# Kernel optimization log

Measured on AMD Instinct MI355X. Metric: run time of the kernel, lower is better.

Reference implementation:

```python
import jax, jax.numpy as jnp
import numpy as np

B, A, S, D, OUT = 8, 16384, 2048, 512, 512
REDUCTION = "mean"  # matches init_kwargs


def setup_inputs() -> dict:
    key = jax.random.key(0)
    k1, k2, k3 = jax.random.split(key, 3)
    input_rep = jax.random.normal(k1, (B, A, D), jnp.float32)
    # sorted residue ids per protein (atoms are stored residue-by-residue)
    aa_res_ids = jnp.sort(jax.random.randint(k2, (B, A), 0, S), axis=-1).astype(jnp.int32)
    input_aa_len = jnp.full((B,), A, jnp.int32)
    input_seq_len = jnp.full((B,), S, jnp.int32)
    W = jax.random.normal(k3, (OUT, D), jnp.float32) / np.sqrt(D)
    bias = jnp.zeros((OUT,), jnp.float32)
    return {"input_rep": input_rep, "aa_res_ids": aa_res_ids,
            "input_aa_len": input_aa_len, "input_seq_len": input_seq_len,
            "W": W, "bias": bias}


def _pool(input_rep, aa_res_ids, input_aa_len, input_seq_len):
    # input_rep: [B, A, D]; aa_res_ids: [B, A] in [0, S)
    Bv, Av, Dv = input_rep.shape
    valid = jnp.arange(Av)[None, :] < input_aa_len[:, None]          # [B, A] atoms within aa_len
    seg = jnp.arange(Bv)[:, None] * S + aa_res_ids                   # flatten (b, res_id) -> segment id
    seg = jnp.where(valid, seg, Bv * S)                              # invalid atoms -> dummy segment
    nseg = Bv * S + 1
    seg_f = seg.reshape(-1)
    counts = jax.ops.segment_sum(valid.reshape(-1).astype(input_rep.dtype), seg_f,
                                 num_segments=nseg)[: Bv * S].reshape(Bv, S)
    if REDUCTION == "mean":
        sums = jax.ops.segment_sum(input_rep.reshape(Bv * Av, Dv), seg_f,
                                   num_segments=nseg)[: Bv * S].reshape(Bv, S, Dv)
        pooled = sums / jnp.maximum(counts, 1)[..., None]
    elif REDUCTION == "max":
        vals = jnp.where(valid[..., None], input_rep, -jnp.inf).reshape(Bv * Av, Dv)
        pooled = jax.ops.segment_max(vals, seg_f, num_segments=nseg)[: Bv * S].reshape(Bv, S, Dv)
        pooled = jnp.where((counts > 0)[..., None], pooled, 0.0)
    else:
        raise ValueError("Unsupported reduction method: {}".format(REDUCTION))
    in_seq = jnp.arange(S)[None, :] < input_seq_len[:, None]         # [B, S] positions within seq_len
    filled = (counts > 0) & in_seq                                   # residues that received >=1 atom
    n_fill = filled.sum(axis=1)                                      # [B]
    avg = (pooled * filled[..., None]).sum(axis=1) / jnp.maximum(n_fill, 1)[:, None].astype(input_rep.dtype)
    # unfilled-but-in-range positions get the per-protein average of filled residues; out-of-range stay 0
    out = jnp.where(filled[..., None], pooled,
                    jnp.where(in_seq[..., None], avg[:, None, :], jnp.zeros((), input_rep.dtype)))
    return out


def reference(input_rep, aa_res_ids, input_aa_len, input_seq_len, W, bias):
    out = _pool(input_rep, aa_res_ids, input_aa_len, input_seq_len)  # [B, S, D]
    return out @ W.T + bias                                          # [B, S, OUT]
```

## Files before the change

### kernel.cpp

```cpp
#include <hip/hip_runtime.h>
#include <cstdint>
#include <cstddef>

#define Bv 8
#define Av 16384
#define Sv 2048
#define Dv 512
#define OUTv 512
#define Mv (Bv * Sv)

using u16 = unsigned short;
using f32x4 = __attribute__((ext_vector_type(4))) float;
using bf16x8 = __attribute__((ext_vector_type(8))) short;

__device__ __forceinline__ u16 f2bf(float x) {
  union { float f; uint32_t u; } v; v.f = x;
  uint32_t u = v.u;
  uint32_t r = u + 0x7FFFu + ((u >> 16) & 1u);
  return (u16)(r >> 16);
}
__device__ __forceinline__ float bf2f(u16 h) {
  union { uint32_t u; float f; } v; v.u = ((uint32_t)h) << 16; return v.f;
}

__device__ __forceinline__ void gl_lds16(const void* g, void* s) {
  __builtin_amdgcn_global_load_lds(
      (const __attribute__((address_space(1))) unsigned int*)g,
      (__attribute__((address_space(3))) unsigned int*)s, 16, 0, 0);
}

__global__ __launch_bounds__(256)
void starts_kernel(const int* __restrict__ res_ids, const int* __restrict__ aa_len,
                   int* __restrict__ starts) {
  const int b = blockIdx.y;
  const int a = blockIdx.x * 256 + threadIdx.x;
  int alen = aa_len[b];
  alen = alen < 0 ? 0 : (alen > Av ? Av : alen);
  int* st = starts + b * (Sv + 1);
  if (a >= alen) {
    if (a == 0) {
      for (int s = 0; s <= Sv; ++s) st[s] = 0;
    }
    return;
  }
  const int* ids = res_ids + b * Av;
  const int id = ids[a];
  const int p = (a == 0) ? -1 : ids[a - 1];
  for (int s = p + 1; s <= id; ++s) st[s] = a;
  if (a == alen - 1) {
    for (int s = id + 1; s <= Sv; ++s) st[s] = alen;
  }
}

__global__ __launch_bounds__(128)
void pool_kernel(const float* __restrict__ rep, const int* __restrict__ starts,
                 u16* __restrict__ pooled) {
  const int bs = blockIdx.x;
  const int b = bs >> 11;
  const int s = bs & (Sv - 1);
  const int* st = starts + b * (Sv + 1);
  const int start = st[s];
  const int end = st[s + 1];
  const int cnt = end - start;

  const int t = threadIdx.x;
  float p0 = 0.f, p1 = 0.f, p2 = 0.f, p3 = 0.f;
  float q0 = 0.f, q1 = 0.f, q2 = 0.f, q3 = 0.f;
  float r0 = 0.f, r1 = 0.f, r2 = 0.f, r3 = 0.f;
  float w0 = 0.f, w1 = 0.f, w2 = 0.f, w3 = 0.f;
  const float* base = rep + (size_t)b * Av * Dv + t * 4;
  int a = start;
  for (; a + 4 <= end; a += 4) {
    float4 v0 = *(const float4*)(base + (size_t)(a + 0) * Dv);
    float4 v1 = *(const float4*)(base + (size_t)(a + 1) * Dv);
    float4 v2 = *(const float4*)(base + (size_t)(a + 2) * Dv);
    float4 v3 = *(const float4*)(base + (size_t)(a + 3) * Dv);
    p0 += v0.x; p1 += v0.y; p2 += v0.z; p3 += v0.w;
    q0 += v1.x; q1 += v1.y; q2 += v1.z; q3 += v1.w;
    r0 += v2.x; r1 += v2.y; r2 += v2.z; r3 += v2.w;
    w0 += v3.x; w1 += v3.y; w2 += v3.z; w3 += v3.w;
  }
  for (; a < end; ++a) {
    float4 v = *(const float4*)(base + (size_t)a * Dv);
    p0 += v.x; p1 += v.y; p2 += v.z; p3 += v.w;
  }
  p0 += q0 + r0 + w0; p1 += q1 + r1 + w1; p2 += q2 + r2 + w2; p3 += q3 + r3 + w3;
  const float inv = cnt > 0 ? 1.0f / (float)cnt : 0.0f;
  ushort4 o = { f2bf(p0 * inv), f2bf(p1 * inv), f2bf(p2 * inv), f2bf(p3 * inv) };
  *(ushort4*)(pooled + (size_t)bs * Dv + t * 4) = o;
}

__global__ __launch_bounds__(256)
void wconv_kernel(const float* __restrict__ W, u16* __restrict__ Wb) {
  const int i = (blockIdx.x * 256 + threadIdx.x) * 4;
  float4 v = *(const float4*)(W + i);
  ushort4 o = { f2bf(v.x), f2bf(v.y), f2bf(v.z), f2bf(v.w) };
  *(ushort4*)(Wb + i) = o;
}

__global__ __launch_bounds__(128)
void avg_kernel(const u16* __restrict__ pooled, const int* __restrict__ starts,
                const int* __restrict__ seq_len, float* __restrict__ avg_sum,
                int* __restrict__ n_fill) {
  const int b = blockIdx.x;
  const int chunk = blockIdx.y;
  const int t = threadIdx.x;
  int slen = seq_len[b];
  slen = slen < 0 ? 0 : (slen > Sv ? Sv : slen);
  const int* st = starts + b * (Sv + 1);
  const int s0 = chunk * 16;
  float a0 = 0.f, a1 = 0.f, a2 = 0.f, a3 = 0.f;
  int filled = 0;
  for (int s = s0; s < s0 + 16; ++s) {
    if (s < slen && st[s + 1] - st[s] > 0) {
      ++filled;
      ushort4 v = *(const ushort4*)(pooled + ((size_t)(b * Sv + s)) * Dv + t * 4);
      a0 += bf2f(v.x); a1 += bf2f(v.y); a2 += bf2f(v.z); a3 += bf2f(v.w);
    }
  }
  atomicAdd(&avg_sum[b * Dv + t * 4 + 0], a0);
  atomicAdd(&avg_sum[b * Dv + t * 4 + 1], a1);
  atomicAdd(&avg_sum[b * Dv + t * 4 + 2], a2);
  atomicAdd(&avg_sum[b * Dv + t * 4 + 3], a3);
  if (t == 0 && filled > 0) atomicAdd(&n_fill[b], filled);
}

__global__ __launch_bounds__(64)
void fixup_kernel(u16* __restrict__ pooled, const int* __restrict__ starts,
                  const int* __restrict__ seq_len, const float* __restrict__ avg_sum,
                  const int* __restrict__ n_fill) {
  const int bs = blockIdx.x;
  const int b = bs >> 11;
  const int s = bs & (Sv - 1);
  int slen = seq_len[b];
  slen = slen < 0 ? 0 : (slen > Sv ? Sv : slen);
  const int* st = starts + b * (Sv + 1);
  const int cnt = st[s + 1] - st[s];
  const int t = threadIdx.x;
  if (s >= slen) {
    if (cnt != 0) {
      ushort4 z = {0, 0, 0, 0};
      *(ushort4*)(pooled + (size_t)bs * Dv + t * 8) = z;
      *(ushort4*)(pooled + (size_t)bs * Dv + t * 8 + 4) = z;
    }
    return;
  }
  if (cnt > 0) return;
  const int nf = n_fill[b];
  const float inv = 1.0f / (float)(nf > 0 ? nf : 1);
  float4 v0 = *(const float4*)(avg_sum + b * Dv + t * 8);
  float4 v1 = *(const float4*)(avg_sum + b * Dv + t * 8 + 4);
  ushort4 o0 = { f2bf(v0.x * inv), f2bf(v0.y * inv), f2bf(v0.z * inv), f2bf(v0.w * inv) };
  ushort4 o1 = { f2bf(v1.x * inv), f2bf(v1.y * inv), f2bf(v1.z * inv), f2bf(v1.w * inv) };
  *(ushort4*)(pooled + (size_t)bs * Dv + t * 8) = o0;
  *(ushort4*)(pooled + (size_t)bs * Dv + t * 8 + 4) = o1;
}

#define BM 128
#define BN 128
#define BK 64

__global__ __launch_bounds__(256, 2)
void gemm_kernel(const u16* __restrict__ A, const u16* __restrict__ Bw,
                 const float* __restrict__ bias, float* __restrict__ out) {
  __shared__ alignas(16) u16 As[BM * BK];
  __shared__ alignas(16) u16 Bs[BN * BK];
  const int tid = threadIdx.x;
  const int m0 = blockIdx.x * BM;
  const int n0 = blockIdx.y * BN;
  const int lane = tid & 63;
  const int wave = tid >> 6;
  const int wm = (wave & 1) * 64;
  const int wn = (wave >> 1) * 64;
  const int fr = lane & 15;
  const int fq = lane >> 4;

  f32x4 acc[4][4];
#pragma unroll
  for (int i = 0; i < 4; ++i)
#pragma unroll
    for (int j = 0; j < 4; ++j) acc[i][j] = (f32x4){0.f, 0.f, 0.f, 0.f};

  const char* Ab = (const char*)A;
  const char* Bb = (const char*)Bw;

  for (int k0 = 0; k0 < Dv; k0 += BK) {
    __syncthreads();
#pragma unroll
    for (int c = 0; c < 4; ++c) {
      const int off = (c * 256 + tid) * 16;
      const int row = off >> 7;
      const int inb = off & 127;
      gl_lds16(Ab + (size_t)(m0 + row) * (Dv * 2) + k0 * 2 + inb, (char*)As + off);
      gl_lds16(Bb + (size_t)(n0 + row) * (Dv * 2) + k0 * 2 + inb, (char*)Bs + off);
    }
    __syncthreads();

#pragma unroll
    for (int ks = 0; ks < 2; ++ks) {
      bf16x8 af[4], bfv[4];
#pragma unroll
      for (int mi = 0; mi < 4; ++mi)
        af[mi] = *(const bf16x8*)(As + (wm + mi * 16 + fr) * BK + ks * 32 + fq * 8);
#pragma unroll
      for (int ni = 0; ni < 4; ++ni)
        bfv[ni] = *(const bf16x8*)(Bs + (wn + ni * 16 + fr) * BK + ks * 32 + fq * 8);
#pragma unroll
      for (int mi = 0; mi < 4; ++mi)
#pragma unroll
        for (int ni = 0; ni < 4; ++ni)
          acc[mi][ni] = __builtin_amdgcn_mfma_f32_16x16x32_bf16(bfv[ni], af[mi], acc[mi][ni], 0, 0, 0);
    }
  }

#pragma unroll
  for (int mi = 0; mi < 4; ++mi) {
    const int row = m0 + wm + mi * 16 + fr;
#pragma unroll
    for (int ni = 0; ni < 4; ++ni) {
      const int colb = n0 + wn + ni * 16 + fq * 4;
      float4 bv = *(const float4*)(bias + colb);
      f32x4 v = acc[mi][ni];
      float4 o = { v[0] + bv.x, v[1] + bv.y, v[2] + bv.z, v[3] + bv.w };
      *(float4*)(out + (size_t)row * OUTv + colb) = o;
    }
  }
}

extern "C" void kernel_launch(void* const* d_in, const int* in_sizes, int n_in,
                              void* d_out, int out_size, void* d_ws, size_t ws_size,
                              hipStream_t stream) {
  (void)in_sizes; (void)n_in; (void)out_size; (void)ws_size;
  const float* rep     = (const float*)d_in[0];
  const int*   res_ids = (const int*)d_in[1];
  const int*   aa_len  = (const int*)d_in[2];
  const int*   seq_len = (const int*)d_in[3];
  const float* W       = (const float*)d_in[4];
  const float* bias    = (const float*)d_in[5];
  float* out = (float*)d_out;

  char* ws = (char*)d_ws;
  u16*   pooled  = (u16*)ws;
  u16*   Wb      = (u16*)(ws + 16777216);
  int*   starts  = (int*)(ws + 17301504);
  float* avg_sum = (float*)(ws + 17367072);
  int*   n_fill  = (int*)(ws + 17383456);

  hipMemsetAsync(avg_sum, 0, Bv * Dv * sizeof(float) + Bv * sizeof(int), stream);

  wconv_kernel<<<(OUTv * Dv) / (256 * 4), 256, 0, stream>>>(W, Wb);
  starts_kernel<<<dim3(Av / 256, Bv), 256, 0, stream>>>(res_ids, aa_len, starts);
  pool_kernel<<<Mv, 128, 0, stream>>>(rep, starts, pooled);
  avg_kernel<<<dim3(Bv, 128), 128, 0, stream>>>(pooled, starts, seq_len, avg_sum, n_fill);
  fixup_kernel<<<Mv, 64, 0, stream>>>(pooled, starts, seq_len, avg_sum, n_fill);
  gemm_kernel<<<dim3(Mv / BM, OUTv / BN), 256, 0, stream>>>(pooled, Wb, bias, out);
}
```

Measured before the change: 429.3 us.

## Fold avg/zero fixup into GEMM row-source selection and drop memset

Replaces the per-row fixup kernel, which wrote average or zero rows into the pooled buffer, with a small kernel that builds one bf16 average vector per protein plus a zero row. The GEMM now picks each A-row's source pointer (pooled row, average vector or zero row) from the segment starts and seq_len. The hipMemsetAsync is replaced by zeroing inside the weight-conversion kernel, and atomics are skipped for chunks with no filled residues. This removes a launch over all 16K rows and a pass over pooled, at the cost of per-row pointer setup in the GEMM.

```diff
diff --git a/kernel.cpp b/kernel.cpp
--- a/kernel.cpp
+++ b/kernel.cpp
@@ -91,11 +91,20 @@
 }
 
 __global__ __launch_bounds__(256)
-void wconv_kernel(const float* __restrict__ W, u16* __restrict__ Wb) {
+void wconv_kernel(const float* __restrict__ W, u16* __restrict__ Wb,
+                  float* __restrict__ avg_sum, int* __restrict__ n_fill) {
   const int i = (blockIdx.x * 256 + threadIdx.x) * 4;
   float4 v = *(const float4*)(W + i);
   ushort4 o = { f2bf(v.x), f2bf(v.y), f2bf(v.z), f2bf(v.w) };
   *(ushort4*)(Wb + i) = o;
+  if (blockIdx.x == 0) {
+    const int t = threadIdx.x;
+    float4 z4 = {0.f, 0.f, 0.f, 0.f};
+#pragma unroll
+    for (int j = 0; j < (Bv * Dv) / (4 * 256); ++j)
+      *(float4*)(avg_sum + (j * 256 + t) * 4) = z4;
+    if (t < Bv) n_fill[t] = 0;
+  }
 }
 
 __global__ __launch_bounds__(128)
@@ -118,42 +127,29 @@
       a0 += bf2f(v.x); a1 += bf2f(v.y); a2 += bf2f(v.z); a3 += bf2f(v.w);
     }
   }
-  atomicAdd(&avg_sum[b * Dv + t * 4 + 0], a0);
-  atomicAdd(&avg_sum[b * Dv + t * 4 + 1], a1);
-  atomicAdd(&avg_sum[b * Dv + t * 4 + 2], a2);
-  atomicAdd(&avg_sum[b * Dv + t * 4 + 3], a3);
-  if (t == 0 && filled > 0) atomicAdd(&n_fill[b], filled);
-}
-
-__global__ __launch_bounds__(64)
-void fixup_kernel(u16* __restrict__ pooled, const int* __restrict__ starts,
-                  const int* __restrict__ seq_len, const float* __restrict__ avg_sum,
-                  const int* __restrict__ n_fill) {
-  const int bs = blockIdx.x;
-  const int b = bs >> 11;
-  const int s = bs & (Sv - 1);
-  int slen = seq_len[b];
-  slen = slen < 0 ? 0 : (slen > Sv ? Sv : slen);
-  const int* st = starts + b * (Sv + 1);
-  const int cnt = st[s + 1] - st[s];
+  if (filled > 0) {
+    atomicAdd(&avg_sum[b * Dv + t * 4 + 0], a0);
+    atomicAdd(&avg_sum[b * Dv + t * 4 + 1], a1);
+    atomicAdd(&avg_sum[b * Dv + t * 4 + 2], a2);
+    atomicAdd(&avg_sum[b * Dv + t * 4 + 3], a3);
+    if (t == 0) atomicAdd(&n_fill[b], filled);
+  }
+}
+
+__global__ __launch_bounds__(128)
+void avgvec_kernel(const float* __restrict__ avg_sum, const int* __restrict__ n_fill,
+                   u16* __restrict__ avgbf, u16* __restrict__ zrow) {
+  const int b = blockIdx.x;
   const int t = threadIdx.x;
-  if (s >= slen) {
-    if (cnt != 0) {
-      ushort4 z = {0, 0, 0, 0};
-      *(ushort4*)(pooled + (size_t)bs * Dv + t * 8) = z;
-      *(ushort4*)(pooled + (size_t)bs * Dv + t * 8 + 4) = z;
-    }
-    return;
-  }
-  if (cnt > 0) return;
   const int nf = n_fill[b];
   const float inv = 1.0f / (float)(nf > 0 ? nf : 1);
-  float4 v0 = *(const float4*)(avg_sum + b * Dv + t * 8);
-  float4 v1 = *(const float4*)(avg_sum + b * Dv + t * 8 + 4);
-  ushort4 o0 = { f2bf(v0.x * inv), f2bf(v0.y * inv), f2bf(v0.z * inv), f2bf(v0.w * inv) };
-  ushort4 o1 = { f2bf(v1.x * inv), f2bf(v1.y * inv), f2bf(v1.z * inv), f2bf(v1.w * inv) };
-  *(ushort4*)(pooled + (size_t)bs * Dv + t * 8) = o0;
-  *(ushort4*)(pooled + (size_t)bs * Dv + t * 8 + 4) = o1;
+  float4 v = *(const float4*)(avg_sum + b * Dv + t * 4);
+  ushort4 o = { f2bf(v.x * inv), f2bf(v.y * inv), f2bf(v.z * inv), f2bf(v.w * inv) };
+  *(ushort4*)(avgbf + (size_t)b * Dv + t * 4) = o;
+  if (b == 0) {
+    ushort4 z = {0, 0, 0, 0};
+    *(ushort4*)(zrow + t * 4) = z;
+  }
 }
 
 #define BM 128
@@ -162,12 +158,36 @@
 
 __global__ __launch_bounds__(256, 2)
 void gemm_kernel(const u16* __restrict__ A, const u16* __restrict__ Bw,
+                 const int* __restrict__ starts, const int* __restrict__ seq_len,
+                 const u16* __restrict__ avgbf, const u16* __restrict__ zrow,
                  const float* __restrict__ bias, float* __restrict__ out) {
   __shared__ alignas(16) u16 As[BM * BK];
   __shared__ alignas(16) u16 Bs[BN * BK];
   const int tid = threadIdx.x;
   const int m0 = blockIdx.x * BM;
   const int n0 = blockIdx.y * BN;
+  const int b = m0 >> 11;
+  int slen = seq_len[b];
+  slen = slen < 0 ? 0 : (slen > Sv ? Sv : slen);
+  const int* st = starts + b * (Sv + 1);
+
+  const int inb = (tid & 7) * 16;
+  const char* aSrc[4];
+  const char* bSrc[4];
+#pragma unroll
+  for (int c = 0; c < 4; ++c) {
+    const int r = c * 32 + (tid >> 3);
+    const int rm = m0 + r;
+    const int s = rm & (Sv - 1);
+    const int cnt = st[s + 1] - st[s];
+    const u16* src;
+    if (s >= slen)      src = zrow;
+    else if (cnt > 0)   src = A + (size_t)rm * Dv;
+    else                src = avgbf + (size_t)b * Dv;
+    aSrc[c] = (const char*)src + inb;
+    bSrc[c] = (const char*)(Bw + (size_t)(n0 + r) * Dv) + inb;
+  }
+
   const int lane = tid & 63;
   const int wave = tid >> 6;
   const int wm = (wave & 1) * 64;
@@ -181,18 +201,13 @@
 #pragma unroll
     for (int j = 0; j < 4; ++j) acc[i][j] = (f32x4){0.f, 0.f, 0.f, 0.f};
 
-  const char* Ab = (const char*)A;
-  const char* Bb = (const char*)Bw;
-
   for (int k0 = 0; k0 < Dv; k0 += BK) {
     __syncthreads();
 #pragma unroll
     for (int c = 0; c < 4; ++c) {
       const int off = (c * 256 + tid) * 16;
-      const int row = off >> 7;
-      const int inb = off & 127;
-      gl_lds16(Ab + (size_t)(m0 + row) * (Dv * 2) + k0 * 2 + inb, (char*)As + off);
-      gl_lds16(Bb + (size_t)(n0 + row) * (Dv * 2) + k0 * 2 + inb, (char*)Bs + off);
+      gl_lds16(aSrc[c] + k0 * 2, (char*)As + off);
+      gl_lds16(bSrc[c] + k0 * 2, (char*)Bs + off);
     }
     __syncthreads();
 
@@ -245,13 +260,14 @@
   int*   starts  = (int*)(ws + 17301504);
   float* avg_sum = (float*)(ws + 17367072);
   int*   n_fill  = (int*)(ws + 17383456);
-
-  hipMemsetAsync(avg_sum, 0, Bv * Dv * sizeof(float) + Bv * sizeof(int), stream);
-
-  wconv_kernel<<<(OUTv * Dv) / (256 * 4), 256, 0, stream>>>(W, Wb);
+  u16*   avgbf   = (u16*)(ws + 17383488);
+  u16*   zrow    = (u16*)(ws + 17391680);
+
+  wconv_kernel<<<(OUTv * Dv) / (256 * 4), 256, 0, stream>>>(W, Wb, avg_sum, n_fill);
   starts_kernel<<<dim3(Av / 256, Bv), 256, 0, stream>>>(res_ids, aa_len, starts);
   pool_kernel<<<Mv, 128, 0, stream>>>(rep, starts, pooled);
   avg_kernel<<<dim3(Bv, 128), 128, 0, stream>>>(pooled, starts, seq_len, avg_sum, n_fill);
-  fixup_kernel<<<Mv, 64, 0, stream>>>(pooled, starts, seq_len, avg_sum, n_fill);
-  gemm_kernel<<<dim3(Mv / BM, OUTv / BN), 256, 0, stream>>>(pooled, Wb, bias, out);
-}
+  avgvec_kernel<<<Bv, 128, 0, stream>>>(avg_sum, n_fill, avgbf, zrow);
+  gemm_kernel<<<dim3(Mv / BM, OUTv / BN), 256, 0, stream>>>(
+      pooled, Wb, starts, seq_len, avgbf, zrow, bias, out);
+}
```

Result: no change. 425.0 us (-1.0%).
